# Kernel tuning notes

Measured on AMD Instinct MI355X. Metric: run time of the kernel, lower is better.

## Reference

```python
import jax, jax.numpy as jnp
import numpy as np

B, T, D, H = 4, 2048, 512, 8
DH = D // H  # 64
EPS = 1e-5


def setup_inputs() -> dict:
    key = jax.random.key(0)
    ks = jax.random.split(key, 12)
    s = lambda k, shp, fan: jax.random.normal(k, shp, jnp.float32) * (fan ** -0.5)
    return {
        "x": jax.random.normal(ks[0], (B, T, D), jnp.float32),
        "ln1_g": jnp.ones((D,), jnp.float32),
        "ln1_b": jnp.zeros((D,), jnp.float32),
        "Wq": s(ks[1], (H, D, DH), D),  # per-head bias-free projections
        "Wk": s(ks[2], (H, D, DH), D),
        "Wv": s(ks[3], (H, D, DH), D),
        "Wproj": s(ks[4], (D, D), D),
        "bproj": jnp.zeros((D,), jnp.float32),
        "W1": s(ks[5], (D, 4 * D), D),
        "b1": jnp.zeros((4 * D,), jnp.float32),
        "W2": s(ks[6], (4 * D, D), 4 * D),
        "b2": jnp.zeros((D,), jnp.float32),
    }


def _layernorm(x, g, b):
    m = jnp.mean(x, axis=-1, keepdims=True)
    v = jnp.var(x, axis=-1, keepdims=True)
    return (x - m) * jax.lax.rsqrt(v + EPS) * g + b


def reference(x, ln1_g, ln1_b, Wq, Wk, Wv, Wproj, bproj, W1, b1, W2, b2):
    b, t, c = x.shape
    scale = c ** -0.5  # source scales by input channel dim, not head_size
    causal = jnp.tril(jnp.ones((t, t), bool))  # [T,T]

    # --- attention sublayer (pre-norm with ln1) ---
    h = _layernorm(x, ln1_g, ln1_b)
    q = jnp.einsum('btd,hde->bhte', h, Wq)
    k = jnp.einsum('btd,hde->bhte', h, Wk)
    v = jnp.einsum('btd,hde->bhte', h, Wv)
    scores = jnp.einsum('bhte,bhse->bhts', q, k) * scale  # [B,H,T,T]
    scores = jnp.where(causal, scores, -jnp.inf)
    att = jax.nn.softmax(scores, axis=-1)  # dropout = identity at inference
    o = jnp.einsum('bhts,bhse->bthe', att, v).reshape(b, t, c)  # concat heads
    sa = o @ Wproj + bproj
    x = x + sa

    # --- FFN sublayer (source reuses ln1, faithful) ---
    h2 = _layernorm(x, ln1_g, ln1_b)
    ff = jax.nn.relu(h2 @ W1 + b1) @ W2 + b2
    return x + ff
```

## Files before the change

kernel.cpp:

```cpp
#include <hip/hip_runtime.h>
#include <math.h>

#define B_ 4
#define T_ 2048
#define D_ 512
#define H_ 8
#define DH_ 64
#define BT_ 8192
#define FF_ 2048
#define EPS_ 1e-5f
#define SCALE_ 0.04419417382415922f
#define SC2_ 0.06375861151f
#define NEGINF_ -1e30f

typedef short b16x8 __attribute__((ext_vector_type(8)));
typedef short b16x4 __attribute__((ext_vector_type(4)));
typedef float f32x4 __attribute__((ext_vector_type(4)));

#define MFMA16(a, b, c) __builtin_amdgcn_mfma_f32_16x16x32_bf16(a, b, c, 0, 0, 0)
#define MFMA16K16(a, b, c) __builtin_amdgcn_mfma_f32_16x16x16bf16_1k(a, b, c, 0, 0, 0)

#define GLL16(gp, lp) \
    __builtin_amdgcn_global_load_lds((const __attribute__((address_space(1))) void*)(gp), \
                                     (__attribute__((address_space(3))) void*)(lp), 16, 0, 0)

#if __has_builtin(__builtin_amdgcn_exp2f)
#define EXP2F(x) __builtin_amdgcn_exp2f(x)
#else
#define EXP2F(x) exp2f(x)
#endif

static __device__ inline short f2bf(float f) {
    unsigned int u = __builtin_bit_cast(unsigned int, f);
    unsigned int r = (u + 0x7fffu + ((u >> 16) & 1u)) >> 16;
    return (short)r;
}
static __device__ inline short f2bf_trunc(float f) {
    return (short)(__builtin_bit_cast(unsigned int, f) >> 16);
}
static __device__ inline float bf2f(short s) {
    return __builtin_bit_cast(float, ((unsigned int)(unsigned short)s) << 16);
}

__global__ __launch_bounds__(256) void prologue_kernel(
        const float* __restrict__ Wq, const float* __restrict__ Wk,
        const float* __restrict__ Wv, const float* __restrict__ Wp,
        const float* __restrict__ W1, const float* __restrict__ W2,
        short* __restrict__ wqkv, short* __restrict__ wpt,
        short* __restrict__ w1t, short* __restrict__ w2t,
        const float* __restrict__ X, const float* __restrict__ G,
        const float* __restrict__ Bb, short* __restrict__ Y)
{
    __shared__ float tile[32][33];
    int idx = blockIdx.x;
    if (idx >= 3072) {
        int tid = threadIdx.y * 32 + threadIdx.x;
        int wave = tid >> 6, t = tid & 63;
        int row = (idx - 3072) * 4 + wave;
        const float* xr = X + (size_t)row * D_;
        float4 v0 = *(const float4*)(xr + t * 4);
        float4 v1 = *(const float4*)(xr + 256 + t * 4);
        float sum = v0.x + v0.y + v0.z + v0.w + v1.x + v1.y + v1.z + v1.w;
        float ssq = v0.x*v0.x + v0.y*v0.y + v0.z*v0.z + v0.w*v0.w
                  + v1.x*v1.x + v1.y*v1.y + v1.z*v1.z + v1.w*v1.w;
        #pragma unroll
        for (int off = 32; off > 0; off >>= 1) {
            sum += __shfl_down(sum, off);
            ssq += __shfl_down(ssq, off);
        }
        sum = __shfl(sum, 0);
        ssq = __shfl(ssq, 0);
        float mean = sum * (1.0f / D_);
        float var  = ssq * (1.0f / D_) - mean * mean;
        float rstd = rsqrtf(var + EPS_);
        float4 g0 = *(const float4*)(G + t * 4);
        float4 g1 = *(const float4*)(G + 256 + t * 4);
        float4 b0 = *(const float4*)(Bb + t * 4);
        float4 b1 = *(const float4*)(Bb + 256 + t * 4);
        short4 o0, o1;
        o0.x = f2bf((v0.x - mean) * rstd * g0.x + b0.x);
        o0.y = f2bf((v0.y - mean) * rstd * g0.y + b0.y);
        o0.z = f2bf((v0.z - mean) * rstd * g0.z + b0.z);
        o0.w = f2bf((v0.w - mean) * rstd * g0.w + b0.w);
        o1.x = f2bf((v1.x - mean) * rstd * g1.x + b1.x);
        o1.y = f2bf((v1.y - mean) * rstd * g1.y + b1.y);
        o1.z = f2bf((v1.z - mean) * rstd * g1.z + b1.z);
        o1.w = f2bf((v1.w - mean) * rstd * g1.w + b1.w);
        short* yr = Y + (size_t)row * D_;
        *(short4*)(yr + t * 4)       = o0;
        *(short4*)(yr + 256 + t * 4) = o1;
        return;
    }
    const float* src; short* dst; int R, C, tx0, ty0;
    if (idx < 768) {
        int w = idx >> 8, rem = idx & 255;
        int hh = rem >> 5, t = rem & 31;
        const float* base = (w == 0) ? Wq : ((w == 1) ? Wk : Wv);
        src = base + hh * (D_ * DH_);
        dst = wqkv + w * (512 * 512) + hh * (DH_ * D_);
        R = 512; C = 64; tx0 = (t & 1) * 32; ty0 = (t >> 1) * 32;
    } else if (idx < 1024) {
        int t = idx - 768;
        src = Wp; dst = wpt; R = 512; C = 512;
        tx0 = (t & 15) * 32; ty0 = (t >> 4) * 32;
    } else if (idx < 2048) {
        int t = idx - 1024;
        src = W1; dst = w1t; R = 512; C = 2048;
        tx0 = (t & 63) * 32; ty0 = (t >> 6) * 32;
    } else {
        int t = idx - 2048;
        src = W2; dst = w2t; R = 2048; C = 512;
        tx0 = (t & 15) * 32; ty0 = (t >> 4) * 32;
    }
    int tx = threadIdx.x, ty = threadIdx.y;
    #pragma unroll
    for (int i = 0; i < 32; i += 8)
        tile[ty + i][tx] = src[(size_t)(ty0 + ty + i) * C + tx0 + tx];
    __syncthreads();
    #pragma unroll
    for (int i = 0; i < 32; i += 8)
        dst[(size_t)(tx0 + ty + i) * R + ty0 + tx] = f2bf(tile[tx][ty + i]);
}

__global__ __launch_bounds__(256) void ln_bf16_kernel(const short* __restrict__ X,
        const float* __restrict__ G, const float* __restrict__ Bb,
        short* __restrict__ Y)
{
    int wave = threadIdx.x >> 6, t = threadIdx.x & 63;
    int row = blockIdx.x * 4 + wave;
    const short* xr = X + (size_t)row * D_ + t * 8;
    b16x8 xv = *(const b16x8*)xr;
    float v[8];
    float sum = 0.0f, ssq = 0.0f;
    #pragma unroll
    for (int e = 0; e < 8; ++e) {
        v[e] = bf2f(xv[e]);
        sum += v[e];
        ssq += v[e] * v[e];
    }
    #pragma unroll
    for (int off = 32; off > 0; off >>= 1) {
        sum += __shfl_down(sum, off);
        ssq += __shfl_down(ssq, off);
    }
    sum = __shfl(sum, 0);
    ssq = __shfl(ssq, 0);
    float mean = sum * (1.0f / D_);
    float var  = ssq * (1.0f / D_) - mean * mean;
    float rstd = rsqrtf(var + EPS_);

    float4 g0 = *(const float4*)(G + t * 8);
    float4 g1 = *(const float4*)(G + t * 8 + 4);
    float4 b0 = *(const float4*)(Bb + t * 8);
    float4 b1 = *(const float4*)(Bb + t * 8 + 4);
    float gg[8] = {g0.x, g0.y, g0.z, g0.w, g1.x, g1.y, g1.z, g1.w};
    float bb[8] = {b0.x, b0.y, b0.z, b0.w, b1.x, b1.y, b1.z, b1.w};
    b16x8 o;
    #pragma unroll
    for (int e = 0; e < 8; ++e)
        o[e] = f2bf((v[e] - mean) * rstd * gg[e] + bb[e]);
    *(b16x8*)(Y + (size_t)row * D_ + t * 8) = o;
}

__global__ __launch_bounds__(256) void mm64_kernel(const short* __restrict__ A,
        const short* __restrict__ Bt, void* __restrict__ C,
        const float* __restrict__ bias, const float* __restrict__ resid,
        int M, int N, int K, int relu, int out_bf16)
{
    __shared__ short As[2][128 * 32];
    __shared__ short Bs[2][64 * 32];
    const int tid = threadIdx.x;
    const int wave = tid >> 6, lane = tid & 63;
    const int quad = lane >> 4, l15 = lane & 15;
    const int m0 = blockIdx.x * 128, n0 = blockIdx.y * 64;
    const int mw = (wave & 1) * 64, nw = (wave >> 1) * 32;

#define STAGE_M64(bufi, kk) \
    { \
        for (int r = 0; r < 2; ++r) { \
            int c = r * 256 + tid; \
            int row = c >> 2, seg = (c & 3) ^ ((row >> 1) & 3); \
            GLL16(A + (size_t)(m0 + row) * K + (kk) + seg * 8, \
                  As[bufi] + (size_t)(r * 256 + wave * 64) * 8); \
        } \
        { \
            int row = tid >> 2, seg = (tid & 3) ^ ((row >> 1) & 3); \
            GLL16(Bt + (size_t)(n0 + row) * K + (kk) + seg * 8, \
                  Bs[bufi] + (size_t)(wave * 64) * 8); \
        } \
    }

    f32x4 acc[4][2];
    #pragma unroll
    for (int i = 0; i < 4; ++i)
        #pragma unroll
        for (int j = 0; j < 2; ++j)
            acc[i][j] = (f32x4){0.f, 0.f, 0.f, 0.f};

    STAGE_M64(0, 0);
    int buf = 0;
    for (int k0 = 0; k0 < K; k0 += 32) {
        __syncthreads();
        if (k0 + 32 < K) STAGE_M64(buf ^ 1, k0 + 32);
        b16x8 af[4], bf[2];
        #pragma unroll
        for (int i = 0; i < 4; ++i) {
            int row = mw + i * 16 + l15;
            af[i] = *(const b16x8*)(As[buf] + row * 32 + ((quad ^ ((row >> 1) & 3)) * 8));
        }
        #pragma unroll
        for (int j = 0; j < 2; ++j) {
            int row = nw + j * 16 + l15;
            bf[j] = *(const b16x8*)(Bs[buf] + row * 32 + ((quad ^ ((row >> 1) & 3)) * 8));
        }
        #pragma unroll
        for (int i = 0; i < 4; ++i)
            #pragma unroll
            for (int j = 0; j < 2; ++j)
                acc[i][j] = MFMA16(af[i], bf[j], acc[i][j]);
        buf ^= 1;
    }
#undef STAGE_M64

    #pragma unroll
    for (int i = 0; i < 4; ++i) {
        #pragma unroll
        for (int r = 0; r < 4; ++r) {
            size_t row = (size_t)(m0 + mw + i * 16 + quad * 4 + r);
            #pragma unroll
            for (int j = 0; j < 2; ++j) {
                int col = n0 + nw + j * 16 + l15;
                float v = acc[i][j][r];
                if (bias)  v += bias[col];
                if (resid) v += resid[row * N + col];
                if (relu)  v = fmaxf(v, 0.0f);
                if (out_bf16) ((short*)C)[row * N + col] = f2bf(v);
                else          ((float*)C)[row * N + col] = v;
            }
        }
    }
}

__global__ __launch_bounds__(256) void mm6464_kernel(const short* __restrict__ A,
        const short* __restrict__ Bt, void* __restrict__ C,
        const float* __restrict__ bias, const void* __restrict__ resid,
        int M, int N, int K, int relu, int out_bf16, int resid_bf16)
{
    __shared__ short As[2][64 * 64];
    __shared__ short Bs[2][64 * 64];
    const int tid = threadIdx.x;
    const int wave = tid >> 6, lane = tid & 63;
    const int quad = lane >> 4, l15 = lane & 15;
    const int m0 = blockIdx.x * 64, n0 = blockIdx.y * 64;
    const int nw = wave * 16;

#define STAGE_M66(bufi, kk) \
    { \
        for (int r = 0; r < 2; ++r) { \
            int c = r * 256 + tid; \
            int row = c >> 3, seg = (c & 7) ^ (row & 7); \
            GLL16(A + (size_t)(m0 + row) * K + (kk) + seg * 8, \
                  As[bufi] + (size_t)(r * 256 + wave * 64) * 8); \
            GLL16(Bt + (size_t)(n0 + row) * K + (kk) + seg * 8, \
                  Bs[bufi] + (size_t)(r * 256 + wave * 64) * 8); \
        } \
    }

    f32x4 acc[4];
    #pragma unroll
    for (int i = 0; i < 4; ++i) acc[i] = (f32x4){0.f, 0.f, 0.f, 0.f};

    STAGE_M66(0, 0);
    int buf = 0;
    for (int k0 = 0; k0 < K; k0 += 64) {
        __syncthreads();
        if (k0 + 64 < K) STAGE_M66(buf ^ 1, k0 + 64);
        b16x8 af[4][2], bf[2];
        #pragma unroll
        for (int i = 0; i < 4; ++i)
            #pragma unroll
            for (int kb = 0; kb < 2; ++kb) {
                int row = i * 16 + l15;
                af[i][kb] = *(const b16x8*)(As[buf] + row * 64 + (((kb * 4 + quad) ^ (row & 7)) * 8));
            }
        #pragma unroll
        for (int kb = 0; kb < 2; ++kb) {
            int row = nw + l15;
            bf[kb] = *(const b16x8*)(Bs[buf] + row * 64 + (((kb * 4 + quad) ^ (row & 7)) * 8));
        }
        #pragma unroll
        for (int kb = 0; kb < 2; ++kb)
            #pragma unroll
            for (int i = 0; i < 4; ++i)
                acc[i] = MFMA16(af[i][kb], bf[kb], acc[i]);
        buf ^= 1;
    }
#undef STAGE_M66

    #pragma unroll
    for (int i = 0; i < 4; ++i) {
        #pragma unroll
        for (int r = 0; r < 4; ++r) {
            size_t row = (size_t)(m0 + i * 16 + quad * 4 + r);
            int col = n0 + nw + l15;
            float v = acc[i][r];
            if (bias)  v += bias[col];
            if (resid) {
                if (resid_bf16) v += bf2f(((const short*)resid)[row * N + col]);
                else            v += ((const float*)resid)[row * N + col];
            }
            if (relu)  v = fmaxf(v, 0.0f);
            if (out_bf16) ((short*)C)[row * N + col] = f2bf(v);
            else          ((float*)C)[row * N + col] = v;
        }
    }
}

__global__ __launch_bounds__(256) void attn_kernel(const short* __restrict__ qkv,
        short* __restrict__ Opart, float* __restrict__ Ml)
{
    __shared__ short Qs[64 * 64];
    __shared__ short Ks[2][64 * 64];
    __shared__ short Vt[2][64 * 64];

    const int tid = threadIdx.x;
    const int wave = tid >> 6, lane = tid & 63;
    const int quad = lane >> 4, l15 = lane & 15;
    const int bh = blockIdx.x;
    const int qi = 31 - (int)blockIdx.y;
    const int split = blockIdx.z;
    const int b = bh >> 3, h = bh & 7;
    const size_t tok0 = (size_t)b * T_;
    const int qrow_rel = wave * 16 + l15;
    const int half = (qi + 1) >> 1;
    const int klo = split ? half : 0;
    const int khi = split ? qi + 1 : half;
    const int pidx = split * 1024 + bh * 32 + qi;
    short* Op = Opart + (size_t)pidx * 4096;
    float* mlp = Ml + (size_t)pidx * 64;

    if (klo >= khi) {
        for (int i = tid; i < 2048; i += 256) ((int*)Op)[i] = 0;
        if (tid < 64) mlp[tid] = 0.0f;
        return;
    }

    const int s_ = tid >> 5, tp = tid & 31;
    const int gg = tp >> 1, hlf = tp & 1;
    const short* vbase = qkv + (tok0 + tp * 2) * 1536 + 1024 + h * 64 + s_ * 8;

    b16x8 v0 = *(const b16x8*)(vbase + (size_t)klo * 64 * 1536);
    b16x8 v1 = *(const b16x8*)(vbase + (size_t)klo * 64 * 1536 + 1536);
    #pragma unroll
    for (int r = 0; r < 2; ++r) {
        int c = r * 256 + tid;
        int tk = c >> 3;
        int seg = (c & 7) ^ (tk & 7);
        GLL16(qkv + (tok0 + qi * 64 + tk) * 1536 + h * 64 + seg * 8,
              Qs + (size_t)(r * 256 + wave * 64) * 8);
        GLL16(qkv + (tok0 + klo * 64 + tk) * 1536 + 512 + h * 64 + seg * 8,
              Ks[0] + (size_t)(r * 256 + wave * 64) * 8);
    }
    {
        int* vo = (int*)Vt[0];
        #pragma unroll
        for (int e = 0; e < 8; ++e) {
            int row = s_ * 8 + e;
            unsigned int pk = (unsigned int)(unsigned short)v0[e]
                            | ((unsigned int)(unsigned short)v1[e] << 16);
            vo[row * 32 + ((gg ^ (row & 15)) << 1) + hlf] = pk;
        }
    }
    {
        int kv1 = (klo + 1 < khi) ? klo + 1 : klo;
        v0 = *(const b16x8*)(vbase + (size_t)kv1 * 64 * 1536);
        v1 = *(const b16x8*)(vbase + (size_t)kv1 * 64 * 1536 + 1536);
    }

    float lrow = 0.0f;
    f32x4 ot[4];
    #pragma unroll
    for (int dt = 0; dt < 4; ++dt) ot[dt] = (f32x4){0.f, 0.f, 0.f, 0.f};

    __syncthreads();

    b16x8 qf[2];
    #pragma unroll
    for (int kb = 0; kb < 2; ++kb) {
        int row = wave * 16 + l15;
        qf[kb] = *(const b16x8*)(Qs + row * 64 + (((kb * 4 + quad) ^ (row & 7)) * 8));
    }

    int cur = 0;
    for (int kj = klo; kj < khi; ++kj, cur ^= 1) {
        f32x4 st[4];
        #pragma unroll
        for (int mt = 0; mt < 4; ++mt) st[mt] = (f32x4){0.f, 0.f, 0.f, 0.f};
        #pragma unroll
        for (int mt = 0; mt < 4; ++mt) {
            int trow = mt * 16 + l15;
            #pragma unroll
            for (int kb = 0; kb < 2; ++kb) {
                b16x8 kf = *(const b16x8*)(Ks[cur] + trow * 64 + (((kb * 4 + quad) ^ (trow & 7)) * 8));
                st[mt] = MFMA16(kf, qf[kb], st[mt]);
            }
        }

        if (kj + 1 < khi) {
            #pragma unroll
            for (int r = 0; r < 2; ++r) {
                int c = r * 256 + tid;
                int tk = c >> 3;
                int seg = (c & 7) ^ (tk & 7);
                GLL16(qkv + (tok0 + (kj + 1) * 64 + tk) * 1536 + 512 + h * 64 + seg * 8,
                      Ks[cur ^ 1] + (size_t)(r * 256 + wave * 64) * 8);
            }
            int* vo = (int*)Vt[cur ^ 1];
            #pragma unroll
            for (int e = 0; e < 8; ++e) {
                int row = s_ * 8 + e;
                unsigned int pk = (unsigned int)(unsigned short)v0[e]
                                | ((unsigned int)(unsigned short)v1[e] << 16);
                vo[row * 32 + ((gg ^ (row & 15)) << 1) + hlf] = pk;
            }
            if (kj + 2 < khi) {
                v0 = *(const b16x8*)(vbase + (size_t)(kj + 2) * 64 * 1536);
                v1 = *(const b16x8*)(vbase + (size_t)(kj + 2) * 64 * 1536 + 1536);
            }
        }

        const bool diag = (kj == qi);
        float rs = 0.0f;
        b16x4 pf[4];
        #pragma unroll
        for (int mt = 0; mt < 4; ++mt)
            #pragma unroll
            for (int r = 0; r < 4; ++r) {
                float sv = st[mt][r];
                if (diag && (mt * 16 + quad * 4 + r) > qrow_rel) sv = NEGINF_;
                float e = EXP2F(sv * SC2_);
                rs += e;
                pf[mt][r] = f2bf_trunc(e);
            }
        rs += __shfl_xor(rs, 16);
        rs += __shfl_xor(rs, 32);
        lrow += rs;

        #pragma unroll
        for (int dt = 0; dt < 4; ++dt) {
            const short* vrow = Vt[cur] + (dt * 16 + l15) * 64;
            #pragma unroll
            for (int kt = 0; kt < 4; ++kt) {
                b16x4 vf = *(const b16x4*)(vrow + (((kt * 4 + quad) ^ l15) << 2));
                ot[dt] = MFMA16K16(vf, pf[kt], ot[dt]);
            }
        }

        __syncthreads();
    }

    float inv = 1.0f / lrow;
    short* strip = (short*)Ks;
    #pragma unroll
    for (int dt = 0; dt < 4; ++dt) {
        b16x4 o4;
        o4[0] = f2bf(ot[dt][0] * inv);
        o4[1] = f2bf(ot[dt][1] * inv);
        o4[2] = f2bf(ot[dt][2] * inv);
        o4[3] = f2bf(ot[dt][3] * inv);
        *(b16x4*)(strip + (size_t)qrow_rel * 72 + dt * 16 + quad * 4) = o4;
    }
    {
        int row = tid >> 2, ch = tid & 3;
        b16x8 lo = *(const b16x8*)(strip + (size_t)row * 72 + ch * 16);
        b16x8 hi = *(const b16x8*)(strip + (size_t)row * 72 + ch * 16 + 8);
        short* dst = Op + row * 64 + ch * 16;
        *(b16x8*)dst = lo;
        *(b16x8*)(dst + 8) = hi;
    }
    if (quad == 0) mlp[qrow_rel] = lrow;
}

__global__ __launch_bounds__(256) void attn_combine_kernel(
        const short* __restrict__ Opart, const float* __restrict__ Ml,
        short* __restrict__ Ob)
{
    int pair = blockIdx.x;
    int bh = pair >> 5, qi = pair & 31;
    int b = bh >> 3, h = bh & 7;
    int tid = threadIdx.x;
    const short* O1 = Opart + (size_t)pair * 4096;
    const short* O2 = Opart + (size_t)(1024 + pair) * 4096;
    const float* ml1 = Ml + (size_t)pair * 64;
    const float* ml2 = Ml + (size_t)(1024 + pair) * 64;
    int ch = tid & 7;
    #pragma unroll
    for (int it = 0; it < 2; ++it) {
        int row = it * 32 + (tid >> 3);
        float l1 = ml1[row], l2 = ml2[row];
        float inv = 1.0f / (l1 + l2);
        float w1 = l1 * inv, w2 = l2 * inv;
        b16x8 a = *(const b16x8*)(O1 + row * 64 + ch * 8);
        b16x8 c = *(const b16x8*)(O2 + row * 64 + ch * 8);
        b16x8 o;
        #pragma unroll
        for (int e = 0; e < 8; ++e)
            o[e] = f2bf(w1 * bf2f(a[e]) + w2 * bf2f(c[e]));
        short* dst = Ob + ((size_t)(b * T_ + qi * 64 + row)) * 512 + h * 64 + ch * 8;
        *(b16x8*)dst = o;
    }
}

extern "C" void kernel_launch(void* const* d_in, const int* in_sizes, int n_in,
                              void* d_out, int out_size, void* d_ws, size_t ws_size,
                              hipStream_t stream) {
    (void)in_sizes; (void)n_in; (void)out_size; (void)ws_size;
    const float* x     = (const float*)d_in[0];
    const float* ln_g  = (const float*)d_in[1];
    const float* ln_b  = (const float*)d_in[2];
    const float* Wq    = (const float*)d_in[3];
    const float* Wk    = (const float*)d_in[4];
    const float* Wv    = (const float*)d_in[5];
    const float* Wproj = (const float*)d_in[6];
    const float* bproj = (const float*)d_in[7];
    const float* W1    = (const float*)d_in[8];
    const float* b1    = (const float*)d_in[9];
    const float* W2    = (const float*)d_in[10];
    const float* b2    = (const float*)d_in[11];
    float* out = (float*)d_out;

    char* W = (char*)d_ws;
    short* hbuf  = (short*)(W + 0);
    short* qkvb  = (short*)(W + ((size_t)8  << 20));
    short* attno = (short*)(W + ((size_t)32 << 20));
    short* x1b   = (short*)(W + ((size_t)40 << 20));
    short* ff1   = (short*)(W + ((size_t)56 << 20));
    short* wqkv  = (short*)(W + ((size_t)88 << 20));
    short* wpt   = (short*)(W + ((size_t)90 << 20));
    short* w1t   = (short*)(W + ((size_t)91 << 20));
    short* w2t   = (short*)(W + ((size_t)93 << 20));
    short* Opart = (short*)(W + ((size_t)96 << 20));
    float* Ml    = (float*)(W + ((size_t)112 << 20));

    prologue_kernel<<<dim3(3072 + BT_ / 4), dim3(32, 8), 0, stream>>>(
        Wq, Wk, Wv, Wproj, W1, W2, wqkv, wpt, w1t, w2t,
        x, ln_g, ln_b, hbuf);
    mm64_kernel<<<dim3(64, 24), dim3(256), 0, stream>>>(hbuf, wqkv, qkvb,
        nullptr, nullptr, BT_, 1536, D_, 0, 1);
    attn_kernel<<<dim3(32, 32, 2), dim3(256), 0, stream>>>(qkvb, Opart, Ml);
    attn_combine_kernel<<<dim3(1024), dim3(256), 0, stream>>>(Opart, Ml, attno);
    mm6464_kernel<<<dim3(128, 8), dim3(256), 0, stream>>>(attno, wpt, x1b,
        bproj, x, BT_, D_, D_, 0, 1, 0);
    ln_bf16_kernel<<<dim3(BT_ / 4), dim3(256), 0, stream>>>(x1b, ln_g, ln_b, hbuf);
    mm64_kernel<<<dim3(64, 32), dim3(256), 0, stream>>>(hbuf, w1t, ff1,
        b1, nullptr, BT_, FF_, D_, 1, 1);
    mm6464_kernel<<<dim3(128, 8), dim3(256), 0, stream>>>(ff1, w2t, out,
        b2, x1b, BT_, D_, FF_, 0, 0, 1);
}
```

Baseline: 260.5 us.

## Load Q and K fragments directly from global into registers in attention

The attention kernel no longer stages Q and K through shared memory. Each lane now loads its MFMA fragments straight from global memory, and only V is kept in LDS (transposed and double-buffered), along with a dedicated output strip. This lowers LDS use and adds a launch-bounds occupancy hint of 4 blocks, and the barrier moves to the top of the loop. In exchange, K loads become per-lane strided global reads that sit on the critical path before the QK MFMAs, with no prefetch distance, which may expose global latency.

Result: slower. 317.3 us (+21.8%).

```diff
diff --git a/kernel.cpp b/kernel.cpp
--- a/kernel.cpp
+++ b/kernel.cpp
@@ -316,12 +316,11 @@
     }
 }
 
-__global__ __launch_bounds__(256) void attn_kernel(const short* __restrict__ qkv,
+__global__ __launch_bounds__(256, 4) void attn_kernel(const short* __restrict__ qkv,
         short* __restrict__ Opart, float* __restrict__ Ml)
 {
-    __shared__ short Qs[64 * 64];
-    __shared__ short Ks[2][64 * 64];
-    __shared__ short Vt[2][64 * 64];
+    __shared__ short Vt[2][4096];
+    __shared__ short strip[64 * 72];
 
     const int tid = threadIdx.x;
     const int wave = tid >> 6, lane = tid & 63;
@@ -347,19 +346,15 @@
 
     const int s_ = tid >> 5, tp = tid & 31;
     const int gg = tp >> 1, hlf = tp & 1;
-    const short* vbase = qkv + (tok0 + tp * 2) * 1536 + 1024 + h * 64 + s_ * 8;
-
-    b16x8 v0 = *(const b16x8*)(vbase + (size_t)klo * 64 * 1536);
-    b16x8 v1 = *(const b16x8*)(vbase + (size_t)klo * 64 * 1536 + 1536);
-    #pragma unroll
-    for (int r = 0; r < 2; ++r) {
-        int c = r * 256 + tid;
-        int tk = c >> 3;
-        int seg = (c & 7) ^ (tk & 7);
-        GLL16(qkv + (tok0 + qi * 64 + tk) * 1536 + h * 64 + seg * 8,
-              Qs + (size_t)(r * 256 + wave * 64) * 8);
-        GLL16(qkv + (tok0 + klo * 64 + tk) * 1536 + 512 + h * 64 + seg * 8,
-              Ks[0] + (size_t)(r * 256 + wave * 64) * 8);
+    const short* vsrc = qkv + (tok0 + tp * 2) * 1536 + 1024 + h * 64 + s_ * 8;
+
+    b16x8 v0 = *(const b16x8*)(vsrc + (size_t)klo * (64 * 1536));
+    b16x8 v1 = *(const b16x8*)(vsrc + (size_t)klo * (64 * 1536) + 1536);
+    b16x8 qf[2];
+    {
+        const short* qp = qkv + (tok0 + qi * 64 + qrow_rel) * 1536 + h * 64 + quad * 8;
+        qf[0] = *(const b16x8*)(qp);
+        qf[1] = *(const b16x8*)(qp + 32);
     }
     {
         int* vo = (int*)Vt[0];
@@ -371,10 +366,9 @@
             vo[row * 32 + ((gg ^ (row & 15)) << 1) + hlf] = pk;
         }
     }
-    {
-        int kv1 = (klo + 1 < khi) ? klo + 1 : klo;
-        v0 = *(const b16x8*)(vbase + (size_t)kv1 * 64 * 1536);
-        v1 = *(const b16x8*)(vbase + (size_t)kv1 * 64 * 1536 + 1536);
+    if (klo + 1 < khi) {
+        v0 = *(const b16x8*)(vsrc + (size_t)(klo + 1) * (64 * 1536));
+        v1 = *(const b16x8*)(vsrc + (size_t)(klo + 1) * (64 * 1536) + 1536);
     }
 
     float lrow = 0.0f;
@@ -382,39 +376,21 @@
     #pragma unroll
     for (int dt = 0; dt < 4; ++dt) ot[dt] = (f32x4){0.f, 0.f, 0.f, 0.f};
 
-    __syncthreads();
-
-    b16x8 qf[2];
-    #pragma unroll
-    for (int kb = 0; kb < 2; ++kb) {
-        int row = wave * 16 + l15;
-        qf[kb] = *(const b16x8*)(Qs + row * 64 + (((kb * 4 + quad) ^ (row & 7)) * 8));
-    }
+    const short* kp = qkv + (tok0 + (size_t)klo * 64 + l15) * 1536 + 512 + h * 64 + quad * 8;
 
     int cur = 0;
     for (int kj = klo; kj < khi; ++kj, cur ^= 1) {
-        f32x4 st[4];
-        #pragma unroll
-        for (int mt = 0; mt < 4; ++mt) st[mt] = (f32x4){0.f, 0.f, 0.f, 0.f};
-        #pragma unroll
-        for (int mt = 0; mt < 4; ++mt) {
-            int trow = mt * 16 + l15;
-            #pragma unroll
-            for (int kb = 0; kb < 2; ++kb) {
-                b16x8 kf = *(const b16x8*)(Ks[cur] + trow * 64 + (((kb * 4 + quad) ^ (trow & 7)) * 8));
-                st[mt] = MFMA16(kf, qf[kb], st[mt]);
-            }
-        }
+        __syncthreads();
+
+        b16x8 kf[4][2];
+        #pragma unroll
+        for (int mt = 0; mt < 4; ++mt)
+            #pragma unroll
+            for (int kb = 0; kb < 2; ++kb)
+                kf[mt][kb] = *(const b16x8*)(kp + (size_t)mt * (16 * 1536) + kb * 32);
+        kp += 64 * 1536;
 
         if (kj + 1 < khi) {
-            #pragma unroll
-            for (int r = 0; r < 2; ++r) {
-                int c = r * 256 + tid;
-                int tk = c >> 3;
-                int seg = (c & 7) ^ (tk & 7);
-                GLL16(qkv + (tok0 + (kj + 1) * 64 + tk) * 1536 + 512 + h * 64 + seg * 8,
-                      Ks[cur ^ 1] + (size_t)(r * 256 + wave * 64) * 8);
-            }
             int* vo = (int*)Vt[cur ^ 1];
             #pragma unroll
             for (int e = 0; e < 8; ++e) {
@@ -424,10 +400,19 @@
                 vo[row * 32 + ((gg ^ (row & 15)) << 1) + hlf] = pk;
             }
             if (kj + 2 < khi) {
-                v0 = *(const b16x8*)(vbase + (size_t)(kj + 2) * 64 * 1536);
-                v1 = *(const b16x8*)(vbase + (size_t)(kj + 2) * 64 * 1536 + 1536);
-            }
-        }
+                v0 = *(const b16x8*)(vsrc + (size_t)(kj + 2) * (64 * 1536));
+                v1 = *(const b16x8*)(vsrc + (size_t)(kj + 2) * (64 * 1536) + 1536);
+            }
+        }
+
+        f32x4 st[4];
+        #pragma unroll
+        for (int mt = 0; mt < 4; ++mt) st[mt] = (f32x4){0.f, 0.f, 0.f, 0.f};
+        #pragma unroll
+        for (int mt = 0; mt < 4; ++mt)
+            #pragma unroll
+            for (int kb = 0; kb < 2; ++kb)
+                st[mt] = MFMA16(kf[mt][kb], qf[kb], st[mt]);
 
         const bool diag = (kj == qi);
         float rs = 0.0f;
@@ -455,12 +440,9 @@
                 ot[dt] = MFMA16K16(vf, pf[kt], ot[dt]);
             }
         }
-
-        __syncthreads();
     }
 
     float inv = 1.0f / lrow;
-    short* strip = (short*)Ks;
     #pragma unroll
     for (int dt = 0; dt < 4; ++dt) {
         b16x4 o4;
```
